# Performance work log

Measured on AMD Instinct MI355X. Metric: run time of the kernel, lower is better.

The kernel has to match this reference:

```python
import jax, jax.numpy as jnp
import numpy as np
import math

B, L, D = 8, 1024, 1024
H = 16
NS = 8
HD = D // H

def setup_inputs() -> dict:
    key = jax.random.key(0)
    ks = jax.random.split(key, 9)
    s = 1.0 / math.sqrt(D)
    inp = {
        "x": jax.random.normal(ks[0], (B, L, D), dtype=jnp.float32),
        "key_padding_mask": jnp.ones((B, L), dtype=bool),
        "Wq_s": jax.random.normal(ks[1], (D, D), dtype=jnp.float32) * s,
        "Wk_s": jax.random.normal(ks[2], (D, D), dtype=jnp.float32) * s,
        "Wv_s": jax.random.normal(ks[3], (D, D), dtype=jnp.float32) * s,
        "Wq_ns": jax.random.normal(ks[4], (NS, D, D), dtype=jnp.float32) * s,
        "Wk_ns": jax.random.normal(ks[5], (NS, D, D), dtype=jnp.float32) * s,
        "Wv_ns": jax.random.normal(ks[6], (NS, D, D), dtype=jnp.float32) * s,
        "W_out": jax.random.normal(ks[7], (D, D), dtype=jnp.float32) * s,
    }
    return inp

def _mixed_proj(x, W_shared, W_ns):
    # x: [B, L, D]; W_shared: [D, D] (out,in); W_ns: [NS, D, D] (per-position out,in)
    L_s = x.shape[1] - W_ns.shape[0]
    s_proj = jnp.einsum('bld,ed->ble', x[:, :L_s], W_shared)       # shared prefix
    ns_proj = jnp.einsum('bnd,ned->bne', x[:, L_s:], W_ns)          # per-position tail
    return jnp.concatenate([s_proj, ns_proj], axis=1)

def reference(x, key_padding_mask, Wq_s, Wk_s, Wv_s, Wq_ns, Wk_ns, Wv_ns, W_out):
    Bv, Lv, Dv = x.shape
    q = _mixed_proj(x, Wq_s, Wq_ns)  # query_len=None -> full
    k = _mixed_proj(x, Wk_s, Wk_ns)
    v = _mixed_proj(x, Wv_s, Wv_ns)
    # [B, H, L, HD]
    q = q.reshape(Bv, Lv, H, HD).transpose(0, 2, 1, 3)
    k = k.reshape(Bv, Lv, H, HD).transpose(0, 2, 1, 3)
    v = v.reshape(Bv, Lv, H, HD).transpose(0, 2, 1, 3)
    causal = jnp.tril(jnp.ones((Lv, Lv), dtype=bool))               # [L_q, L_k]
    mask = causal[None, :, :] & key_padding_mask[:, None, :]        # [B, L_q, L_k]
    scores = jnp.einsum('bhqd,bhkd->bhqk', q, k) / math.sqrt(HD)
    scores = jnp.where(mask[:, None, :, :], scores, jnp.float32(-1e9))
    attn = jax.nn.softmax(scores, axis=-1)  # dropout is identity in eval
    out = jnp.einsum('bhqk,bhkd->bhqd', attn, v)
    out = out.transpose(0, 2, 1, 3).reshape(Bv, Lv, Dv)
    return jnp.einsum('bld,ed->ble', out, W_out)
```

## Files before the change

### kernel.cpp

```cpp
#include <hip/hip_runtime.h>

#define Bsz  8
#define Lsz  1024
#define Dsz  1024
#define Hh   16
#define HDsz 64
#define NSsz 8
#define LSsz 1016

typedef short  bf16x8 __attribute__((ext_vector_type(8)));
typedef float  f32x4  __attribute__((ext_vector_type(4)));

#define GLB(p) ((const __attribute__((address_space(1))) unsigned int*)(p))
#define LDSP(p) ((__attribute__((address_space(3))) unsigned int*)(p))

__device__ __forceinline__ float bf2f(unsigned short u) {
    union { unsigned int i; float f; } v; v.i = ((unsigned int)u) << 16; return v.f;
}
__device__ __forceinline__ unsigned short f2bf(float f) {
    union { float f; unsigned int i; } v; v.f = f;
    unsigned int x = v.i;
    return (unsigned short)((x + 0x7FFFu + ((x >> 16) & 1u)) >> 16);
}

__global__ __launch_bounds__(256) void cast_kernel(
    const float* __restrict__ x,
    const float* __restrict__ wq, const float* __restrict__ wk,
    const float* __restrict__ wv, const float* __restrict__ wo,
    unsigned short* __restrict__ xb,
    unsigned short* __restrict__ wcat,
    unsigned short* __restrict__ wob)
{
    const size_t NX = 2097152;
    const size_t NW = 262144;
    size_t i = (size_t)blockIdx.x * 256 + threadIdx.x;
    const size_t stride = (size_t)gridDim.x * 256;
    const size_t total = NX + 4 * NW;
    for (; i < total; i += stride) {
        const float* src; unsigned short* dst; size_t off;
        if (i < NX)               { src = x;  dst = xb;             off = i; }
        else if (i < NX + NW)     { src = wq; dst = wcat;           off = i - NX; }
        else if (i < NX + 2 * NW) { src = wk; dst = wcat + 1048576; off = i - NX - NW; }
        else if (i < NX + 3 * NW) { src = wv; dst = wcat + 2097152; off = i - NX - 2 * NW; }
        else                      { src = wo; dst = wob;            off = i - NX - 3 * NW; }
        float4 v = reinterpret_cast<const float4*>(src)[off];
        ushort4 o;
        o.x = f2bf(v.x); o.y = f2bf(v.y); o.z = f2bf(v.z); o.w = f2bf(v.w);
        reinterpret_cast<ushort4*>(dst)[off] = o;
    }
}

__global__ __launch_bounds__(256) void gemm_qkv_kernel(
    const unsigned short* __restrict__ Ab,
    const unsigned short* __restrict__ Wb,
    unsigned short* __restrict__ Qo,
    unsigned short* __restrict__ Ko,
    unsigned short* __restrict__ Vo)
{
    __shared__ __align__(16) unsigned short As[128 * 64];
    __shared__ __align__(16) unsigned short Bs[128 * 64];

    const int tid  = threadIdx.x;
    const int lane = tid & 63;
    const int wave = tid >> 6;
    const int wm   = wave >> 1;
    const int wn   = wave & 1;
    const int lr   = lane & 15;
    const int lq   = lane >> 4;
    const int m0   = blockIdx.y * 128;
    const int n0   = blockIdx.x * 128;

    const int lrow = lane >> 3;
    const int lcol = (lane & 7) << 3;

    f32x4 acc[4][4];
    #pragma unroll
    for (int i = 0; i < 4; ++i)
        #pragma unroll
        for (int j = 0; j < 4; ++j)
            acc[i][j] = (f32x4){0.f, 0.f, 0.f, 0.f};

    for (int k0 = 0; k0 < 1024; k0 += 64) {
        #pragma unroll
        for (int it = 0; it < 4; ++it) {
            int row = it * 32 + wave * 8 + lrow;
            const unsigned short* ga = &Ab[(size_t)(m0 + row) * 1024 + k0 + lcol];
            const unsigned short* gb = &Wb[(size_t)(n0 + row) * 1024 + k0 + lcol];
            __builtin_amdgcn_global_load_lds(GLB(ga), LDSP(&As[it * 2048 + wave * 512]), 16, 0, 0);
            __builtin_amdgcn_global_load_lds(GLB(gb), LDSP(&Bs[it * 2048 + wave * 512]), 16, 0, 0);
        }
        __syncthreads();

        #pragma unroll
        for (int ks = 0; ks < 2; ++ks) {
            bf16x8 af[4], bfr[4];
            #pragma unroll
            for (int i = 0; i < 4; ++i)
                af[i] = *reinterpret_cast<const bf16x8*>(
                    &As[(wm * 64 + i * 16 + lr) * 64 + ks * 32 + lq * 8]);
            #pragma unroll
            for (int j = 0; j < 4; ++j)
                bfr[j] = *reinterpret_cast<const bf16x8*>(
                    &Bs[(wn * 64 + j * 16 + lr) * 64 + ks * 32 + lq * 8]);
            #pragma unroll
            for (int i = 0; i < 4; ++i)
                #pragma unroll
                for (int j = 0; j < 4; ++j)
                    acc[i][j] = __builtin_amdgcn_mfma_f32_16x16x32_bf16(
                        af[i], bfr[j], acc[i][j], 0, 0, 0);
        }
        __syncthreads();
    }

    const int t  = n0 >> 10;
    const int d0 = n0 & 1023;
    unsigned short* Out = (t == 0 ? Qo : t == 1 ? Ko : Vo);
    #pragma unroll
    for (int i = 0; i < 4; ++i) {
        #pragma unroll
        for (int j = 0; j < 4; ++j) {
            int col = d0 + wn * 64 + j * 16 + lr;
            #pragma unroll
            for (int r = 0; r < 4; ++r) {
                int row = m0 + wm * 64 + i * 16 + lq * 4 + r;
                Out[(size_t)row * 1024 + col] = f2bf(acc[i][j][r]);
            }
        }
    }
}

__global__ __launch_bounds__(256) void gemm_obf_kernel(
    const unsigned short* __restrict__ Ab,
    const unsigned short* __restrict__ Wb,
    float* __restrict__ Co)
{
    __shared__ __align__(16) unsigned short As[128 * 64];
    __shared__ __align__(16) unsigned short Bs[128 * 64];

    const int tid  = threadIdx.x;
    const int lane = tid & 63;
    const int wave = tid >> 6;
    const int wm   = wave >> 1;
    const int wn   = wave & 1;
    const int lr   = lane & 15;
    const int lq   = lane >> 4;
    const int m0   = blockIdx.y * 128;
    const int n0   = blockIdx.x * 128;

    const int lrow = lane >> 3;
    const int lcol = (lane & 7) << 3;

    f32x4 acc[4][4];
    #pragma unroll
    for (int i = 0; i < 4; ++i)
        #pragma unroll
        for (int j = 0; j < 4; ++j)
            acc[i][j] = (f32x4){0.f, 0.f, 0.f, 0.f};

    for (int k0 = 0; k0 < 1024; k0 += 64) {
        #pragma unroll
        for (int it = 0; it < 4; ++it) {
            int row = it * 32 + wave * 8 + lrow;
            const unsigned short* ga = &Ab[(size_t)(m0 + row) * 1024 + k0 + lcol];
            const unsigned short* gb = &Wb[(size_t)(n0 + row) * 1024 + k0 + lcol];
            __builtin_amdgcn_global_load_lds(GLB(ga), LDSP(&As[it * 2048 + wave * 512]), 16, 0, 0);
            __builtin_amdgcn_global_load_lds(GLB(gb), LDSP(&Bs[it * 2048 + wave * 512]), 16, 0, 0);
        }
        __syncthreads();

        #pragma unroll
        for (int ks = 0; ks < 2; ++ks) {
            bf16x8 af[4], bfr[4];
            #pragma unroll
            for (int i = 0; i < 4; ++i)
                af[i] = *reinterpret_cast<const bf16x8*>(
                    &As[(wm * 64 + i * 16 + lr) * 64 + ks * 32 + lq * 8]);
            #pragma unroll
            for (int j = 0; j < 4; ++j)
                bfr[j] = *reinterpret_cast<const bf16x8*>(
                    &Bs[(wn * 64 + j * 16 + lr) * 64 + ks * 32 + lq * 8]);
            #pragma unroll
            for (int i = 0; i < 4; ++i)
                #pragma unroll
                for (int j = 0; j < 4; ++j)
                    acc[i][j] = __builtin_amdgcn_mfma_f32_16x16x32_bf16(
                        af[i], bfr[j], acc[i][j], 0, 0, 0);
        }
        __syncthreads();
    }

    #pragma unroll
    for (int i = 0; i < 4; ++i) {
        #pragma unroll
        for (int j = 0; j < 4; ++j) {
            int col = n0 + wn * 64 + j * 16 + lr;
            #pragma unroll
            for (int r = 0; r < 4; ++r) {
                int row = m0 + wm * 64 + i * 16 + lq * 4 + r;
                Co[(size_t)row * 1024 + col] = acc[i][j][r];
            }
        }
    }
}

#define GBM 128
#define GBN 128
#define GBK 64

template <bool A_F32, bool C_F32>
__global__ __launch_bounds__(256) void gemm_bt_kernel(
    const void* __restrict__ Av,
    const float* __restrict__ W,
    void* __restrict__ Cv,
    int M, int N, int K)
{
    __shared__ unsigned short As[GBM][GBK];
    __shared__ unsigned short Ws[GBN][GBK];

    const int tid  = threadIdx.x;
    const int lane = tid & 63;
    const int wave = tid >> 6;
    const int wm   = wave >> 1;
    const int wn   = wave & 1;
    const int lr   = lane & 15;
    const int lq   = lane >> 4;
    const int m0   = blockIdx.y * GBM;
    const int n0   = blockIdx.x * GBN;

    f32x4 acc[4][4];
    #pragma unroll
    for (int i = 0; i < 4; ++i)
        #pragma unroll
        for (int j = 0; j < 4; ++j)
            acc[i][j] = (f32x4){0.f, 0.f, 0.f, 0.f};

    for (int k0 = 0; k0 < K; k0 += GBK) {
        if (A_F32) {
            const float* A = (const float*)Av;
            #pragma unroll
            for (int i = 0; i < 8; ++i) {
                int idx = tid + i * 256;
                int row = idx >> 4;
                int c4  = idx & 15;
                float4 a = *reinterpret_cast<const float4*>(
                    &A[(size_t)(m0 + row) * K + k0 + c4 * 4]);
                ushort4 o;
                o.x = f2bf(a.x); o.y = f2bf(a.y);
                o.z = f2bf(a.z); o.w = f2bf(a.w);
                *reinterpret_cast<ushort4*>(&As[row][c4 * 4]) = o;
            }
        } else {
            const unsigned short* A = (const unsigned short*)Av;
            #pragma unroll
            for (int i = 0; i < 4; ++i) {
                int idx = tid + i * 256;
                int row = idx >> 3;
                int c8  = idx & 7;
                int4 v = *reinterpret_cast<const int4*>(
                    &A[(size_t)(m0 + row) * K + k0 + c8 * 8]);
                *reinterpret_cast<int4*>(&As[row][c8 * 8]) = v;
            }
        }
        #pragma unroll
        for (int i = 0; i < 8; ++i) {
            int idx = tid + i * 256;
            int row = idx >> 4;
            int c4  = idx & 15;
            float4 w = *reinterpret_cast<const float4*>(
                &W[(size_t)(n0 + row) * K + k0 + c4 * 4]);
            ushort4 o;
            o.x = f2bf(w.x); o.y = f2bf(w.y);
            o.z = f2bf(w.z); o.w = f2bf(w.w);
            *reinterpret_cast<ushort4*>(&Ws[row][c4 * 4]) = o;
        }
        __syncthreads();

        #pragma unroll
        for (int ks = 0; ks < 2; ++ks) {
            bf16x8 af[4], bfr[4];
            #pragma unroll
            for (int i = 0; i < 4; ++i)
                af[i] = *reinterpret_cast<const bf16x8*>(
                    &As[wm * 64 + i * 16 + lr][ks * 32 + lq * 8]);
            #pragma unroll
            for (int j = 0; j < 4; ++j)
                bfr[j] = *reinterpret_cast<const bf16x8*>(
                    &Ws[wn * 64 + j * 16 + lr][ks * 32 + lq * 8]);
            #pragma unroll
            for (int i = 0; i < 4; ++i)
                #pragma unroll
                for (int j = 0; j < 4; ++j)
                    acc[i][j] = __builtin_amdgcn_mfma_f32_16x16x32_bf16(
                        af[i], bfr[j], acc[i][j], 0, 0, 0);
        }
        __syncthreads();
    }

    #pragma unroll
    for (int i = 0; i < 4; ++i) {
        #pragma unroll
        for (int j = 0; j < 4; ++j) {
            int col = n0 + wn * 64 + j * 16 + lr;
            #pragma unroll
            for (int r = 0; r < 4; ++r) {
                int row = m0 + wm * 64 + i * 16 + lq * 4 + r;
                if (C_F32) {
                    ((float*)Cv)[(size_t)row * N + col] = acc[i][j][r];
                } else {
                    ((unsigned short*)Cv)[(size_t)row * N + col] = f2bf(acc[i][j][r]);
                }
            }
        }
    }
}

__global__ __launch_bounds__(512) void fixup_kernel(
    const float* __restrict__ x,
    const float* __restrict__ Wq_ns,
    const float* __restrict__ Wk_ns,
    const float* __restrict__ Wv_ns,
    unsigned short* __restrict__ Q,
    unsigned short* __restrict__ Kb,
    unsigned short* __restrict__ V)
{
    const int bid   = blockIdx.x;
    const int wgt   = bid >> 6;
    const int chunk = bid & 63;
    const int proj  = wgt >> 3;
    const int n     = wgt & 7;
    const float* Wns =
        (proj == 0 ? Wq_ns : proj == 1 ? Wk_ns : Wv_ns) + (size_t)n * Dsz * Dsz;
    unsigned short* Out = (proj == 0 ? Q : proj == 1 ? Kb : V);
    const int l    = LSsz + n;
    const int b    = threadIdx.x >> 6;
    const int lane = threadIdx.x & 63;

    const float* xrow = x + ((size_t)b * Lsz + l) * Dsz;
    float4 xr[4];
    #pragma unroll
    for (int i = 0; i < 4; ++i)
        xr[i] = *reinterpret_cast<const float4*>(&xrow[lane * 4 + i * 256]);

    for (int er = 0; er < 16; ++er) {
        const int e = chunk * 16 + er;
        const float* wrow = Wns + (size_t)e * Dsz;
        float s = 0.f;
        #pragma unroll
        for (int i = 0; i < 4; ++i) {
            float4 wv = *reinterpret_cast<const float4*>(&wrow[lane * 4 + i * 256]);
            s += wv.x * xr[i].x + wv.y * xr[i].y
               + wv.z * xr[i].z + wv.w * xr[i].w;
        }
        #pragma unroll
        for (int off = 32; off > 0; off >>= 1) s += __shfl_xor(s, off, 64);
        if (lane == 0) Out[((size_t)b * Lsz + l) * Dsz + e] = f2bf(s);
    }
}

__global__ __launch_bounds__(256, 4) void attn_mfma_kernel(
    const unsigned short* __restrict__ Q,
    const unsigned short* __restrict__ K,
    const unsigned short* __restrict__ V,
    unsigned short* __restrict__ O)
{
    __shared__ __align__(16) unsigned short Klds[2 * 4096];
    __shared__ __align__(16) unsigned short Vtlds[4096];
    __shared__ __align__(16) unsigned short Plds[4][1024];

    const int tid  = threadIdx.x;
    const int lane = tid & 63;
    const int wave = tid >> 6;
    const int lr   = lane & 15;
    const int lq   = lane >> 4;

    const int id = blockIdx.x;
    const int qt = 15 - ((id >> 3) & 15);
    const int bh = ((id >> 7) << 3) | (id & 7);
    const int h  = bh & (Hh - 1);
    const int b  = bh >> 4;
    const int qw = qt * 64 + wave * 16;
    const int nkt = qt + 1;

    const size_t base = (size_t)b * Lsz * Dsz + (size_t)h * HDsz;

    bf16x8 qf[2];
    #pragma unroll
    for (int h2 = 0; h2 < 2; ++h2) {
        bf16x8 t = *reinterpret_cast<const bf16x8*>(
            &Q[base + (size_t)(qw + lr) * Dsz + h2 * 32 + lq * 8]);
        #pragma unroll
        for (int e = 0; e < 8; ++e) {
            float f = bf2f((unsigned short)t[e]) * 0.125f;
            t[e] = (short)f2bf(f);
        }
        qf[h2] = t;
    }

    f32x4 acc[4];
    #pragma unroll
    for (int jd = 0; jd < 4; ++jd) acc[jd] = (f32x4){0.f, 0.f, 0.f, 0.f};
    float m_i[4] = {-1e30f, -1e30f, -1e30f, -1e30f};
    float l_i[4] = {0.f, 0.f, 0.f, 0.f};

    const int krow0 = tid >> 3;
    const int kc8   = tid & 7;
    const int vd0   = (tid & 7) * 8;
    const int vk0   = (tid >> 3) * 2;

    unsigned short* Pw = &Plds[wave][0];
    int4 vq0, vq1;

    #pragma unroll
    for (int it = 0; it < 2; ++it) {
        int row  = it * 32 + krow0;
        int csrc = kc8 ^ (row & 7);
        const unsigned short* ga = &K[base + (size_t)row * Dsz + csrc * 8];
        __builtin_amdgcn_global_load_lds(GLB(ga),
            LDSP(&Klds[it * 2048 + wave * 512]), 16, 0, 0);
    }
    vq0 = *reinterpret_cast<const int4*>(&V[base + (size_t)(vk0 + 0) * Dsz + vd0]);
    vq1 = *reinterpret_cast<const int4*>(&V[base + (size_t)(vk0 + 1) * Dsz + vd0]);

    for (int kt = 0; kt < nkt; ++kt) {
        const int k0 = kt * 64;
        const int kb = (kt & 1) * 4096;

        __syncthreads();

        {
            union { int4 v; unsigned short u[8]; } a, c;
            a.v = vq0; c.v = vq1;
            const int kc  = vk0 >> 3;
            const int klo = vk0 & 7;
            #pragma unroll
            for (int d = 0; d < 8; ++d) {
                int dd  = vd0 + d;
                int idx = dd * 64 + (((kc ^ (dd & 7)) << 3) | klo);
                ushort2 p; p.x = a.u[d]; p.y = c.u[d];
                *reinterpret_cast<ushort2*>(&Vtlds[idx]) = p;
            }
        }
        __syncthreads();

        if (kt + 1 < nkt) {
            const int k0n = k0 + 64;
            #pragma unroll
            for (int it = 0; it < 2; ++it) {
                int row  = it * 32 + krow0;
                int csrc = kc8 ^ (row & 7);
                const unsigned short* ga =
                    &K[base + (size_t)(k0n + row) * Dsz + csrc * 8];
                __builtin_amdgcn_global_load_lds(GLB(ga),
                    LDSP(&Klds[(kb ^ 4096) + it * 2048 + wave * 512]), 16, 0, 0);
            }
            vq0 = *reinterpret_cast<const int4*>(
                &V[base + (size_t)(k0n + vk0 + 0) * Dsz + vd0]);
            vq1 = *reinterpret_cast<const int4*>(
                &V[base + (size_t)(k0n + vk0 + 1) * Dsz + vd0]);
        }

        f32x4 sv[4];
        #pragma unroll
        for (int jt = 0; jt < 4; ++jt) sv[jt] = (f32x4){0.f, 0.f, 0.f, 0.f};

        __builtin_amdgcn_s_setprio(1);
        #pragma unroll
        for (int h2 = 0; h2 < 2; ++h2) {
            const int cs = (((h2 << 2) | lq) ^ (lr & 7)) << 3;
            #pragma unroll
            for (int jt = 0; jt < 4; ++jt) {
                bf16x8 kf = *reinterpret_cast<const bf16x8*>(
                    &Klds[kb + (jt * 16 + lr) * 64 + cs]);
                sv[jt] = __builtin_amdgcn_mfma_f32_16x16x32_bf16(
                    qf[h2], kf, sv[jt], 0, 0, 0);
            }
        }
        __builtin_amdgcn_s_setprio(0);

        if (k0 + 63 > qw) {
            #pragma unroll
            for (int jt = 0; jt < 4; ++jt) {
                int kpos = k0 + jt * 16 + lr;
                #pragma unroll
                for (int r = 0; r < 4; ++r) {
                    int q = qw + lq * 4 + r;
                    if (kpos > q) sv[jt][r] = -1e30f;
                }
            }
        }

        float tm[4], al[4], rs[4];
        #pragma unroll
        for (int r = 0; r < 4; ++r)
            tm[r] = fmaxf(fmaxf(sv[0][r], sv[1][r]), fmaxf(sv[2][r], sv[3][r]));
        #pragma unroll
        for (int off = 1; off < 16; off <<= 1)
            #pragma unroll
            for (int r = 0; r < 4; ++r)
                tm[r] = fmaxf(tm[r], __shfl_xor(tm[r], off, 64));
        #pragma unroll
        for (int r = 0; r < 4; ++r) {
            float nm = fmaxf(m_i[r], tm[r]);
            al[r] = __expf(m_i[r] - nm);
            m_i[r] = nm;
        }
        #pragma unroll
        for (int jt = 0; jt < 4; ++jt)
            #pragma unroll
            for (int r = 0; r < 4; ++r)
                sv[jt][r] = __expf(sv[jt][r] - m_i[r]);
        #pragma unroll
        for (int r = 0; r < 4; ++r)
            rs[r] = (sv[0][r] + sv[1][r]) + (sv[2][r] + sv[3][r]);
        #pragma unroll
        for (int off = 1; off < 16; off <<= 1)
            #pragma unroll
            for (int r = 0; r < 4; ++r)
                rs[r] += __shfl_xor(rs[r], off, 64);
        #pragma unroll
        for (int r = 0; r < 4; ++r) l_i[r] = l_i[r] * al[r] + rs[r];
        #pragma unroll
        for (int jd = 0; jd < 4; ++jd)
            #pragma unroll
            for (int r = 0; r < 4; ++r)
                acc[jd][r] *= al[r];

        #pragma unroll
        for (int jt = 0; jt < 4; ++jt) {
            int kcol  = jt * 16 + lr;
            int chunk = kcol >> 3;
            int elem  = kcol & 7;
            #pragma unroll
            for (int r = 0; r < 4; ++r) {
                int qrow = lq * 4 + r;
                Pw[qrow * 64 + (((chunk ^ (qrow & 7)) << 3) | elem)] =
                    f2bf(sv[jt][r]);
            }
        }

        __builtin_amdgcn_s_setprio(1);
        #pragma unroll
        for (int h2 = 0; h2 < 2; ++h2) {
            const int cs = (((h2 << 2) | lq) ^ (lr & 7)) << 3;
            bf16x8 pf = *reinterpret_cast<const bf16x8*>(&Pw[lr * 64 + cs]);
            #pragma unroll
            for (int jd = 0; jd < 4; ++jd) {
                bf16x8 vf = *reinterpret_cast<const bf16x8*>(
                    &Vtlds[(jd * 16 + lr) * 64 + cs]);
                acc[jd] = __builtin_amdgcn_mfma_f32_16x16x32_bf16(
                    pf, vf, acc[jd], 0, 0, 0);
            }
        }
        __builtin_amdgcn_s_setprio(0);
    }

    float inv[4];
    #pragma unroll
    for (int r = 0; r < 4; ++r) inv[r] = 1.0f / l_i[r];
    #pragma unroll
    for (int jd = 0; jd < 4; ++jd) {
        #pragma unroll
        for (int r = 0; r < 4; ++r) {
            int qrow  = lq * 4 + r;
            int col   = jd * 16 + lr;
            int chunk = col >> 3;
            int elem  = col & 7;
            Pw[qrow * 64 + (((chunk ^ (qrow & 7)) << 3) | elem)] =
                f2bf(acc[jd][r] * inv[r]);
        }
    }
    #pragma unroll
    for (int it2 = 0; it2 < 2; ++it2) {
        int row = it2 * 8 + (lane >> 3);
        int c   = lane & 7;
        const int4 ov = *reinterpret_cast<const int4*>(
            &Pw[row * 64 + ((c ^ (row & 7)) << 3)]);
        *reinterpret_cast<int4*>(&O[base + (size_t)(qw + row) * Dsz + c * 8]) = ov;
    }
}

extern "C" void kernel_launch(void* const* d_in, const int* in_sizes, int n_in,
                              void* d_out, int out_size, void* d_ws, size_t ws_size,
                              hipStream_t stream)
{
    const float* x     = (const float*)d_in[0];
    const float* Wq_s  = (const float*)d_in[2];
    const float* Wk_s  = (const float*)d_in[3];
    const float* Wv_s  = (const float*)d_in[4];
    const float* Wq_ns = (const float*)d_in[5];
    const float* Wk_ns = (const float*)d_in[6];
    const float* Wv_ns = (const float*)d_in[7];
    const float* W_out = (const float*)d_in[8];
    float* out = (float*)d_out;

    const size_t nElem = (size_t)Bsz * Lsz * Dsz;
    unsigned short* Q    = (unsigned short*)d_ws;
    unsigned short* Kb   = Q + nElem;
    unsigned short* V    = Kb + nElem;
    unsigned short* Xb   = V + nElem;
    unsigned short* Wcat = Xb + nElem;
    unsigned short* Wob  = Wcat + 3 * 1048576;
    const size_t need = (4 * nElem + 4 * 1048576) * sizeof(unsigned short);

    if (ws_size >= need) {
        cast_kernel<<<3072, 256, 0, stream>>>(x, Wq_s, Wk_s, Wv_s, W_out,
                                              Xb, Wcat, Wob);
        gemm_qkv_kernel<<<dim3(24, 64), 256, 0, stream>>>(Xb, Wcat, Q, Kb, V);
        fixup_kernel<<<24 * 64, 512, 0, stream>>>(x, Wq_ns, Wk_ns, Wv_ns, Q, Kb, V);
        unsigned short* O = Xb;
        attn_mfma_kernel<<<Bsz * Hh * (Lsz / 64), 256, 0, stream>>>(Q, Kb, V, O);
        gemm_obf_kernel<<<dim3(8, 64), 256, 0, stream>>>(O, Wob, out);
    } else {
        unsigned short* O = Xb;
        dim3 ggrid(Dsz / GBN, (Bsz * Lsz) / GBM);
        gemm_bt_kernel<true, false><<<ggrid, 256, 0, stream>>>(x, Wq_s, Q,  Bsz * Lsz, Dsz, Dsz);
        gemm_bt_kernel<true, false><<<ggrid, 256, 0, stream>>>(x, Wk_s, Kb, Bsz * Lsz, Dsz, Dsz);
        gemm_bt_kernel<true, false><<<ggrid, 256, 0, stream>>>(x, Wv_s, V,  Bsz * Lsz, Dsz, Dsz);
        fixup_kernel<<<24 * 64, 512, 0, stream>>>(x, Wq_ns, Wk_ns, Wv_ns, Q, Kb, V);
        attn_mfma_kernel<<<Bsz * Hh * (Lsz / 64), 256, 0, stream>>>(Q, Kb, V, O);
        gemm_bt_kernel<false, true><<<ggrid, 256, 0, stream>>>(O, W_out, out, Bsz * Lsz, Dsz, Dsz);
    }
}
```

Measured before the change: 389.8 us.

## Triple-buffer GEMM LDS tiles with swizzle and larger 256x128 blocks

Replaces the two single-buffered bf16 GEMM kernels with one templated kernel that uses 256x128 tiles, 8 waves, and a three-stage LDS ring filled by async global_load_lds. Loads for tile t+2 are issued while tile t is computed, with vmcnt waits in place of full syncthreads pairs. LDS columns are XOR-swizzled to reduce bank conflicts, and setprio is raised around the MFMA bursts. The aim is to hide global load latency and raise MFMA utilisation. In exchange it needs much more LDS per block, which may limit occupancy, and it launches fewer blocks.

```diff
diff --git a/kernel.cpp b/kernel.cpp
--- a/kernel.cpp
+++ b/kernel.cpp
@@ -50,156 +50,123 @@
     }
 }
 
-__global__ __launch_bounds__(256) void gemm_qkv_kernel(
+#define STAGE3(tt) do {                                                         \
+    const int _k0 = (tt) * 64;                                                  \
+    unsigned short* _Ad = &As[((tt) % 3) * 16384 + wave * 512];                 \
+    unsigned short* _Bd = &Bs[((tt) % 3) * 8192  + wave * 512];                 \
+    _Pragma("unroll")                                                           \
+    for (int _it = 0; _it < 4; ++_it) {                                         \
+        int _r = _it * 64 + srow;                                               \
+        int _c = sc8 ^ (_r & 7);                                                \
+        __builtin_amdgcn_global_load_lds(                                       \
+            GLB(&Ab[(size_t)(m0 + _r) * 1024 + _k0 + _c * 8]),                  \
+            LDSP(_Ad + _it * 4096), 16, 0, 0);                                  \
+    }                                                                           \
+    _Pragma("unroll")                                                           \
+    for (int _it = 0; _it < 2; ++_it) {                                         \
+        int _r = _it * 64 + srow;                                               \
+        int _c = sc8 ^ (_r & 7);                                                \
+        __builtin_amdgcn_global_load_lds(                                       \
+            GLB(&Wb[(size_t)(n0 + _r) * 1024 + _k0 + _c * 8]),                  \
+            LDSP(_Bd + _it * 4096), 16, 0, 0);                                  \
+    }                                                                           \
+} while (0)
+
+template <bool C_F32, bool SPLIT>
+__global__ __launch_bounds__(512, 2) void gemm3_kernel(
     const unsigned short* __restrict__ Ab,
     const unsigned short* __restrict__ Wb,
-    unsigned short* __restrict__ Qo,
-    unsigned short* __restrict__ Ko,
-    unsigned short* __restrict__ Vo)
+    void* __restrict__ O0, void* __restrict__ O1, void* __restrict__ O2)
 {
-    __shared__ __align__(16) unsigned short As[128 * 64];
-    __shared__ __align__(16) unsigned short Bs[128 * 64];
+    __shared__ __align__(16) unsigned short As[3 * 256 * 64];
+    __shared__ __align__(16) unsigned short Bs[3 * 128 * 64];
 
     const int tid  = threadIdx.x;
     const int lane = tid & 63;
     const int wave = tid >> 6;
-    const int wm   = wave >> 1;
-    const int wn   = wave & 1;
+    const int wm   = wave >> 2;
+    const int wn   = wave & 3;
     const int lr   = lane & 15;
     const int lq   = lane >> 4;
-    const int m0   = blockIdx.y * 128;
+    const int m0   = blockIdx.y * 256;
     const int n0   = blockIdx.x * 128;
 
-    const int lrow = lane >> 3;
-    const int lcol = (lane & 7) << 3;
-
-    f32x4 acc[4][4];
-    #pragma unroll
-    for (int i = 0; i < 4; ++i)
-        #pragma unroll
-        for (int j = 0; j < 4; ++j)
+    const int srow = tid >> 3;
+    const int sc8  = tid & 7;
+
+    f32x4 acc[8][2];
+    #pragma unroll
+    for (int i = 0; i < 8; ++i)
+        #pragma unroll
+        for (int j = 0; j < 2; ++j)
             acc[i][j] = (f32x4){0.f, 0.f, 0.f, 0.f};
 
-    for (int k0 = 0; k0 < 1024; k0 += 64) {
-        #pragma unroll
-        for (int it = 0; it < 4; ++it) {
-            int row = it * 32 + wave * 8 + lrow;
-            const unsigned short* ga = &Ab[(size_t)(m0 + row) * 1024 + k0 + lcol];
-            const unsigned short* gb = &Wb[(size_t)(n0 + row) * 1024 + k0 + lcol];
-            __builtin_amdgcn_global_load_lds(GLB(ga), LDSP(&As[it * 2048 + wave * 512]), 16, 0, 0);
-            __builtin_amdgcn_global_load_lds(GLB(gb), LDSP(&Bs[it * 2048 + wave * 512]), 16, 0, 0);
-        }
-        __syncthreads();
-
+    STAGE3(0);
+    STAGE3(1);
+
+    for (int t = 0; t < 16; ++t) {
+        if (t < 15) asm volatile("s_waitcnt vmcnt(6)" ::: "memory");
+        else        asm volatile("s_waitcnt vmcnt(0)" ::: "memory");
+        asm volatile("s_barrier" ::: "memory");
+        if (t + 2 < 16) STAGE3(t + 2);
+
+        const unsigned short* Abuf = &As[(t % 3) * 16384];
+        const unsigned short* Bbuf = &Bs[(t % 3) * 8192];
         #pragma unroll
         for (int ks = 0; ks < 2; ++ks) {
-            bf16x8 af[4], bfr[4];
-            #pragma unroll
-            for (int i = 0; i < 4; ++i)
+            bf16x8 af[8], bfr[2];
+            #pragma unroll
+            for (int i = 0; i < 8; ++i) {
+                int row = wm * 128 + i * 16 + lr;
                 af[i] = *reinterpret_cast<const bf16x8*>(
-                    &As[(wm * 64 + i * 16 + lr) * 64 + ks * 32 + lq * 8]);
-            #pragma unroll
-            for (int j = 0; j < 4; ++j)
+                    &Abuf[row * 64 + (((ks * 4 + lq) ^ (row & 7)) << 3)]);
+            }
+            #pragma unroll
+            for (int j = 0; j < 2; ++j) {
+                int row = wn * 32 + j * 16 + lr;
                 bfr[j] = *reinterpret_cast<const bf16x8*>(
-                    &Bs[(wn * 64 + j * 16 + lr) * 64 + ks * 32 + lq * 8]);
-            #pragma unroll
-            for (int i = 0; i < 4; ++i)
+                    &Bbuf[row * 64 + (((ks * 4 + lq) ^ (row & 7)) << 3)]);
+            }
+            __builtin_amdgcn_s_setprio(1);
+            #pragma unroll
+            for (int i = 0; i < 8; ++i)
                 #pragma unroll
-                for (int j = 0; j < 4; ++j)
+                for (int j = 0; j < 2; ++j)
                     acc[i][j] = __builtin_amdgcn_mfma_f32_16x16x32_bf16(
                         af[i], bfr[j], acc[i][j], 0, 0, 0);
-        }
-        __syncthreads();
-    }
-
-    const int t  = n0 >> 10;
-    const int d0 = n0 & 1023;
-    unsigned short* Out = (t == 0 ? Qo : t == 1 ? Ko : Vo);
-    #pragma unroll
-    for (int i = 0; i < 4; ++i) {
-        #pragma unroll
-        for (int j = 0; j < 4; ++j) {
-            int col = d0 + wn * 64 + j * 16 + lr;
-            #pragma unroll
-            for (int r = 0; r < 4; ++r) {
-                int row = m0 + wm * 64 + i * 16 + lq * 4 + r;
-                Out[(size_t)row * 1024 + col] = f2bf(acc[i][j][r]);
-            }
-        }
-    }
-}
-
-__global__ __launch_bounds__(256) void gemm_obf_kernel(
-    const unsigned short* __restrict__ Ab,
-    const unsigned short* __restrict__ Wb,
-    float* __restrict__ Co)
-{
-    __shared__ __align__(16) unsigned short As[128 * 64];
-    __shared__ __align__(16) unsigned short Bs[128 * 64];
-
-    const int tid  = threadIdx.x;
-    const int lane = tid & 63;
-    const int wave = tid >> 6;
-    const int wm   = wave >> 1;
-    const int wn   = wave & 1;
-    const int lr   = lane & 15;
-    const int lq   = lane >> 4;
-    const int m0   = blockIdx.y * 128;
-    const int n0   = blockIdx.x * 128;
-
-    const int lrow = lane >> 3;
-    const int lcol = (lane & 7) << 3;
-
-    f32x4 acc[4][4];
-    #pragma unroll
-    for (int i = 0; i < 4; ++i)
-        #pragma unroll
-        for (int j = 0; j < 4; ++j)
-            acc[i][j] = (f32x4){0.f, 0.f, 0.f, 0.f};
-
-    for (int k0 = 0; k0 < 1024; k0 += 64) {
-        #pragma unroll
-        for (int it = 0; it < 4; ++it) {
-            int row = it * 32 + wave * 8 + lrow;
-            const unsigned short* ga = &Ab[(size_t)(m0 + row) * 1024 + k0 + lcol];
-            const unsigned short* gb = &Wb[(size_t)(n0 + row) * 1024 + k0 + lcol];
-            __builtin_amdgcn_global_load_lds(GLB(ga), LDSP(&As[it * 2048 + wave * 512]), 16, 0, 0);
-            __builtin_amdgcn_global_load_lds(GLB(gb), LDSP(&Bs[it * 2048 + wave * 512]), 16, 0, 0);
-        }
-        __syncthreads();
-
-        #pragma unroll
-        for (int ks = 0; ks < 2; ++ks) {
-            bf16x8 af[4], bfr[4];
-            #pragma unroll
-            for (int i = 0; i < 4; ++i)
-                af[i] = *reinterpret_cast<const bf16x8*>(
-                    &As[(wm * 64 + i * 16 + lr) * 64 + ks * 32 + lq * 8]);
-            #pragma unroll
-            for (int j = 0; j < 4; ++j)
-                bfr[j] = *reinterpret_cast<const bf16x8*>(
-                    &Bs[(wn * 64 + j * 16 + lr) * 64 + ks * 32 + lq * 8]);
-            #pragma unroll
-            for (int i = 0; i < 4; ++i)
+            __builtin_amdgcn_s_setprio(0);
+        }
+    }
+
+    if (SPLIT) {
+        const int tsel = n0 >> 10;
+        const int d0   = n0 & 1023;
+        unsigned short* Out =
+            (unsigned short*)(tsel == 0 ? O0 : tsel == 1 ? O1 : O2);
+        #pragma unroll
+        for (int i = 0; i < 8; ++i)
+            #pragma unroll
+            for (int j = 0; j < 2; ++j) {
+                int col = d0 + wn * 32 + j * 16 + lr;
                 #pragma unroll
-                for (int j = 0; j < 4; ++j)
-                    acc[i][j] = __builtin_amdgcn_mfma_f32_16x16x32_bf16(
-                        af[i], bfr[j], acc[i][j], 0, 0, 0);
-        }
-        __syncthreads();
-    }
-
-    #pragma unroll
-    for (int i = 0; i < 4; ++i) {
-        #pragma unroll
-        for (int j = 0; j < 4; ++j) {
-            int col = n0 + wn * 64 + j * 16 + lr;
-            #pragma unroll
-            for (int r = 0; r < 4; ++r) {
-                int row = m0 + wm * 64 + i * 16 + lq * 4 + r;
-                Co[(size_t)row * 1024 + col] = acc[i][j][r];
-            }
-        }
+                for (int r = 0; r < 4; ++r) {
+                    int row = m0 + wm * 128 + i * 16 + lq * 4 + r;
+                    Out[(size_t)row * 1024 + col] = f2bf(acc[i][j][r]);
+                }
+            }
+    } else {
+        float* Co = (float*)O0;
+        #pragma unroll
+        for (int i = 0; i < 8; ++i)
+            #pragma unroll
+            for (int j = 0; j < 2; ++j) {
+                int col = n0 + wn * 32 + j * 16 + lr;
+                #pragma unroll
+                for (int r = 0; r < 4; ++r) {
+                    int row = m0 + wm * 128 + i * 16 + lq * 4 + r;
+                    Co[(size_t)row * 1024 + col] = acc[i][j][r];
+                }
+            }
     }
 }
 
@@ -605,11 +572,13 @@
     if (ws_size >= need) {
         cast_kernel<<<3072, 256, 0, stream>>>(x, Wq_s, Wk_s, Wv_s, W_out,
                                               Xb, Wcat, Wob);
-        gemm_qkv_kernel<<<dim3(24, 64), 256, 0, stream>>>(Xb, Wcat, Q, Kb, V);
+        gemm3_kernel<false, true><<<dim3(24, 32), 512, 0, stream>>>(
+            Xb, Wcat, Q, Kb, V);
         fixup_kernel<<<24 * 64, 512, 0, stream>>>(x, Wq_ns, Wk_ns, Wv_ns, Q, Kb, V);
         unsigned short* O = Xb;
         attn_mfma_kernel<<<Bsz * Hh * (Lsz / 64), 256, 0, stream>>>(Q, Kb, V, O);
-        gemm_obf_kernel<<<dim3(8, 64), 256, 0, stream>>>(O, Wob, out);
+        gemm3_kernel<true, false><<<dim3(8, 32), 512, 0, stream>>>(
+            O, Wob, out, nullptr, nullptr);
     } else {
         unsigned short* O = Xb;
         dim3 ggrid(Dsz / GBN, (Bsz * Lsz) / GBM);
```

Result: no change. 388.0 us (-0.5%).
